# Optimization experiments

Measured on AMD Instinct MI355X. Metric: run time of the kernel, lower is better.

Reference implementation:

```python
import jax, jax.numpy as jnp
import numpy as np

N = 30000      # nodes
E = 480000     # edges per relation (avg degree 16)
H = 4          # GAT heads
D = 64         # out_size per head
F1, F2 = 256, 128   # per-metapath input feature dims
SIN = 256      # sen_in_size
HD = H * D     # 256, semantic-attention in_size
OUT = 64       # final out_size


def _gat(feat, src, dst, W, al, ar, b):
    """DGL GATConv (eval mode, dropout=0), activation=relu6."""
    h = (feat @ W).reshape(N, H, D)                     # [N,H,D]
    el = (h * al).sum(-1)                               # [N,H]
    er = (h * ar).sum(-1)                               # [N,H]
    e = jax.nn.leaky_relu(el[src] + er[dst], 0.2)       # [E,H]
    m = jax.ops.segment_max(e, dst, N)                  # edge-softmax over incoming edges
    p = jnp.exp(e - m[dst])
    s = jax.ops.segment_sum(p, dst, N)
    a = p / s[dst]                                      # [E,H]
    out = jax.ops.segment_sum(a[:, :, None] * h[src], dst, N)  # [N,H,D]
    out = out + b.reshape(1, H, D)
    return jnp.clip(out, 0.0, 6.0).reshape(N, H * D)    # relu6, flatten(1)


def _gcn_layer(x, src, dst, W, b):
    """DGL GraphConv, norm='both': D_in^{-1/2} A D_out^{-1/2} X W (+ b)."""
    ones = jnp.ones(src.shape[0], x.dtype)
    deg_o = jnp.clip(jax.ops.segment_sum(ones, src, N), 1.0, None)
    deg_i = jnp.clip(jax.ops.segment_sum(ones, dst, N), 1.0, None)
    h = (x @ W) * (deg_o[:, None] ** -0.5)
    h = jax.ops.segment_sum(h[src], dst, N) * (deg_i[:, None] ** -0.5)
    return h if b is None else h + b


def setup_inputs():
    key = jax.random.key(0)
    ks = jax.random.split(key, 28)
    f32 = jnp.float32
    nrm = lambda k, shp: jax.random.normal(k, shp, f32) * 0.05
    ri = lambda k, shp: jax.random.randint(k, shp, 0, N, jnp.int32)
    return dict(
        feat0=jax.random.normal(ks[0], (N, F1), f32),
        feat1=jax.random.normal(ks[1], (N, F2), f32),
        sen_feat=jax.random.normal(ks[2], (N, SIN), f32),
        Wgat0=nrm(ks[11], (F1, H * D)), al0=nrm(ks[12], (H, D)), ar0=nrm(ks[13], (H, D)), b0=nrm(ks[14], (H * D,)),
        Wgat1=nrm(ks[15], (F2, H * D)), al1=nrm(ks[16], (H, D)), ar1=nrm(ks[17], (H, D)), b1=nrm(ks[18], (H * D,)),
        Wp1=nrm(ks[19], (HD, OUT)), bp1=nrm(ks[20], (OUT,)), wp2=nrm(ks[21], (OUT,)),
        Wf=nrm(ks[22], (HD, OUT)), bf=nrm(ks[23], (OUT,)),
        Wg1=nrm(ks[24], (SIN, OUT)), bg1=nrm(ks[25], (OUT,)), Wg2=nrm(ks[26], (OUT, OUT)),
        src0=ri(ks[3], (E,)), dst0=ri(ks[4], (E,)),
        src1=ri(ks[5], (E,)), dst1=ri(ks[6], (E,)),
        gsrc=ri(ks[7], (E,)), gdst=ri(ks[8], (E,)),
        asrc=ri(ks[9], (E,)), adst=ri(ks[10], (E,)),
        k=10,
    )


def reference(feat0, feat1, sen_feat,
              Wgat0, al0, ar0, b0, Wgat1, al1, ar1, b1,
              Wp1, bp1, wp2, Wf, bf, Wg1, bg1, Wg2,
              src0, dst0, src1, dst1, gsrc, gdst, asrc, adst, k):
    # per-metapath GAT embeddings
    z0 = _gat(feat0, src0, dst0, Wgat0, al0, ar0, b0)   # [N, HD]
    z1 = _gat(feat1, src1, dst1, Wgat1, al1, ar1, b1)   # [N, HD]
    z = jnp.stack([z0, z1], axis=1)                     # [N, M=2, HD]
    # PathAttention (semantic attention over metapaths)
    w = jnp.tanh(z @ Wp1 + bp1) @ wp2                   # [N, M]
    beta = jax.nn.softmax(w.mean(0))                    # [M]
    fused = jnp.einsum('m,nmf->nf', beta, z)            # [N, HD]
    Femb = fused @ Wf + bf                              # [N, OUT]
    # two-layer GCN on the sentence graph
    p1 = jnp.tanh(_gcn_layer(sen_feat, gsrc, gdst, Wg1, bg1))
    P = _gcn_layer(p1, gsrc, gdst, Wg2, None)           # [N, OUT]
    # spectral loss: fuse embeddings, trace of Laplacian quadratic form on first k dims
    Z = 0.5 * (Femb + P)                                # [N, OUT]
    Zk = Z[:, :k]
    diff = Zk[asrc] - Zk[adst]
    tr = 0.5 * jnp.sum(diff * diff)                     # tr(Zk^T (D - A) Zk)
    return (tr, Z)
```

## Files before the change

kernel.cpp:

```cpp
#include <hip/hip_runtime.h>
#include <math.h>

#define NN 30000
#define NE 480000
#define NBLK 118
#define NMT 235
#define NTRB 7500
#define CAPD 128

typedef unsigned short ushort_t;
typedef unsigned int uint_t;
typedef __attribute__((ext_vector_type(8))) short short8;
typedef __attribute__((ext_vector_type(4))) float f32x4;

__device__ __forceinline__ ushort_t f2bf(float x) {
  uint_t u = __float_as_uint(x);
  u = (u + 0x7FFF + ((u >> 16) & 1)) >> 16;
  return (ushort_t)u;
}
__device__ __forceinline__ float bf2f(ushort_t v) {
  return __uint_as_float(((uint_t)v) << 16);
}

__device__ __forceinline__ float wred(float v) {
#pragma unroll
  for (int off = 32; off > 0; off >>= 1) v += __shfl_xor(v, off);
  return v;
}

__global__ void prep_kernel(float4* __restrict__ zp, const float* __restrict__ W0,
                            const float* __restrict__ W1, const float* __restrict__ W2,
                            const float* __restrict__ W3, const float* __restrict__ W4,
                            ushort_t* __restrict__ T0, ushort_t* __restrict__ T1,
                            ushort_t* __restrict__ T2, ushort_t* __restrict__ T3,
                            ushort_t* __restrict__ T4) {
  int id = blockIdx.x * 256 + threadIdx.x;
  if (id < 52501) {
    zp[id] = make_float4(0.f, 0.f, 0.f, 0.f);
    return;
  }
  int wid = id - 52501;
  const float* W;
  ushort_t* T;
  int K, N, base;
  if (wid < 65536) { W = W0; T = T0; K = 256; N = 256; base = 0; }
  else if (wid < 98304) { W = W1; T = T1; K = 128; N = 256; base = 65536; }
  else if (wid < 114688) { W = W2; T = T2; K = 256; N = 64; base = 98304; }
  else if (wid < 131072) { W = W3; T = T3; K = 256; N = 64; base = 114688; }
  else if (wid < 147456) { W = W4; T = T4; K = 256; N = 64; base = 131072; }
  else return;
  int l = wid - base;
  int k = l / N, n = l - k * N;
  T[(size_t)n * K + k] = f2bf(W[l]);
}


__device__ __forceinline__ void mfma_core_f32(const float* __restrict__ A0,
                                              const ushort_t* __restrict__ BT, int K, int bm,
                                              short* __restrict__ As, short* __restrict__ Bs,
                                              f32x4 acc[2][4]) {
  int tid = threadIdx.x;
  int lane = tid & 63, w = tid >> 6;
  int q = lane >> 4, mr = lane & 15;
#pragma unroll 1
  for (int k0 = 0; k0 < K; k0 += 32) {
    {
      int r = tid >> 1, hf = tid & 1;
      int gr = bm + r;
      float4 f0 = make_float4(0.f, 0.f, 0.f, 0.f), f1 = f0, f2 = f0, f3 = f0;
      if (gr < NN) {
        const float4* pa = (const float4*)(A0 + (size_t)gr * K + k0 + hf * 16);
        f0 = pa[0]; f1 = pa[1]; f2 = pa[2]; f3 = pa[3];
      }
      short8 lo, hi;
      lo[0] = (short)f2bf(f0.x); lo[1] = (short)f2bf(f0.y);
      lo[2] = (short)f2bf(f0.z); lo[3] = (short)f2bf(f0.w);
      lo[4] = (short)f2bf(f1.x); lo[5] = (short)f2bf(f1.y);
      lo[6] = (short)f2bf(f1.z); lo[7] = (short)f2bf(f1.w);
      hi[0] = (short)f2bf(f2.x); hi[1] = (short)f2bf(f2.y);
      hi[2] = (short)f2bf(f2.z); hi[3] = (short)f2bf(f2.w);
      hi[4] = (short)f2bf(f3.x); hi[5] = (short)f2bf(f3.y);
      hi[6] = (short)f2bf(f3.z); hi[7] = (short)f2bf(f3.w);
      short* dst = As + r * 40 + hf * 16;
      *(short8*)(dst) = lo;
      *(short8*)(dst + 8) = hi;
    }
    {
      int n = tid >> 2, qk = tid & 3;
      short8 bv = *(const short8*)((const short*)BT + (size_t)n * K + k0 + qk * 8);
      *(short8*)(Bs + n * 40 + qk * 8) = bv;
    }
    __syncthreads();
    short8 a0 = *(short8*)(As + (w * 32 + mr) * 40 + q * 8);
    short8 a1 = *(short8*)(As + (w * 32 + 16 + mr) * 40 + q * 8);
#pragma unroll
    for (int j = 0; j < 4; ++j) {
      short8 b = *(short8*)(Bs + (j * 16 + mr) * 40 + q * 8);
      acc[0][j] = __builtin_amdgcn_mfma_f32_16x16x32_bf16(a0, b, acc[0][j], 0, 0, 0);
      acc[1][j] = __builtin_amdgcn_mfma_f32_16x16x32_bf16(a1, b, acc[1][j], 0, 0, 0);
    }
    __syncthreads();
  }
}

__device__ __forceinline__ void mfma_core2_f32(const float* __restrict__ A0,
                                               const ushort_t* __restrict__ BT, int K, int bm,
                                               short* __restrict__ As, short* __restrict__ Bs,
                                               f32x4 acc[2][8]) {
  int tid = threadIdx.x;
  int lane = tid & 63, w = tid >> 6;
  int q = lane >> 4, mr = lane & 15;
#pragma unroll 1
  for (int k0 = 0; k0 < K; k0 += 32) {
    {
      int r = tid >> 1, hf = tid & 1;
      int gr = bm + r;
      float4 f0 = make_float4(0.f, 0.f, 0.f, 0.f), f1 = f0, f2 = f0, f3 = f0;
      if (gr < NN) {
        const float4* pa = (const float4*)(A0 + (size_t)gr * K + k0 + hf * 16);
        f0 = pa[0]; f1 = pa[1]; f2 = pa[2]; f3 = pa[3];
      }
      short8 lo, hi;
      lo[0] = (short)f2bf(f0.x); lo[1] = (short)f2bf(f0.y);
      lo[2] = (short)f2bf(f0.z); lo[3] = (short)f2bf(f0.w);
      lo[4] = (short)f2bf(f1.x); lo[5] = (short)f2bf(f1.y);
      lo[6] = (short)f2bf(f1.z); lo[7] = (short)f2bf(f1.w);
      hi[0] = (short)f2bf(f2.x); hi[1] = (short)f2bf(f2.y);
      hi[2] = (short)f2bf(f2.z); hi[3] = (short)f2bf(f2.w);
      hi[4] = (short)f2bf(f3.x); hi[5] = (short)f2bf(f3.y);
      hi[6] = (short)f2bf(f3.z); hi[7] = (short)f2bf(f3.w);
      short* dst = As + r * 40 + hf * 16;
      *(short8*)(dst) = lo;
      *(short8*)(dst + 8) = hi;
    }
    {
      int n = tid >> 1, qk = tid & 1;
      const short* src = (const short*)BT + (size_t)n * K + k0 + qk * 16;
      short8 b0 = *(const short8*)src;
      short8 b1 = *(const short8*)(src + 8);
      short* d = Bs + n * 40 + qk * 16;
      *(short8*)d = b0;
      *(short8*)(d + 8) = b1;
    }
    __syncthreads();
    short8 a0 = *(short8*)(As + (w * 32 + mr) * 40 + q * 8);
    short8 a1 = *(short8*)(As + (w * 32 + 16 + mr) * 40 + q * 8);
#pragma unroll
    for (int j = 0; j < 8; ++j) {
      short8 b = *(short8*)(Bs + (j * 16 + mr) * 40 + q * 8);
      acc[0][j] = __builtin_amdgcn_mfma_f32_16x16x32_bf16(a0, b, acc[0][j], 0, 0, 0);
      acc[1][j] = __builtin_amdgcn_mfma_f32_16x16x32_bf16(a1, b, acc[1][j], 0, 0, 0);
    }
    __syncthreads();
  }
}

__device__ __forceinline__ void mfma_core2_bf(const ushort_t* __restrict__ A0,
                                              const ushort_t* __restrict__ BT, int bm,
                                              short* __restrict__ As, short* __restrict__ Bs,
                                              f32x4 acc[2][8]) {
  int tid = threadIdx.x;
  int lane = tid & 63, w = tid >> 6;
  int q = lane >> 4, mr = lane & 15;
#pragma unroll 1
  for (int k0 = 0; k0 < 256; k0 += 32) {
    {
      int r = tid >> 1, hf = tid & 1;
      int gr = bm + r;
      short8 v0 = {0, 0, 0, 0, 0, 0, 0, 0}, v1 = v0;
      if (gr < NN) {
        const short* p0 = (const short*)A0 + (size_t)gr * 256 + k0 + hf * 16;
        v0 = *(const short8*)p0;
        v1 = *(const short8*)(p0 + 8);
      }
      short* dst = As + r * 40 + hf * 16;
      *(short8*)(dst) = v0;
      *(short8*)(dst + 8) = v1;
    }
    {
      int n = tid >> 1, qk = tid & 1;
      const short* src = (const short*)BT + (size_t)n * 256 + k0 + qk * 16;
      short8 b0 = *(const short8*)src;
      short8 b1 = *(const short8*)(src + 8);
      short* d = Bs + n * 40 + qk * 16;
      *(short8*)d = b0;
      *(short8*)(d + 8) = b1;
    }
    __syncthreads();
    short8 a0 = *(short8*)(As + (w * 32 + mr) * 40 + q * 8);
    short8 a1 = *(short8*)(As + (w * 32 + 16 + mr) * 40 + q * 8);
#pragma unroll
    for (int j = 0; j < 8; ++j) {
      short8 b = *(short8*)(Bs + (j * 16 + mr) * 40 + q * 8);
      acc[0][j] = __builtin_amdgcn_mfma_f32_16x16x32_bf16(a0, b, acc[0][j], 0, 0, 0);
      acc[1][j] = __builtin_amdgcn_mfma_f32_16x16x32_bf16(a1, b, acc[1][j], 0, 0, 0);
    }
    __syncthreads();
  }
}

__global__ __launch_bounds__(256) void mfma_all_kernel(
    const float* __restrict__ feat0, const float* __restrict__ feat1,
    const float* __restrict__ sen, const ushort_t* __restrict__ WT0,
    const ushort_t* __restrict__ WT1, const ushort_t* __restrict__ Wg1T,
    ushort_t* __restrict__ h0, ushort_t* __restrict__ h1, ushort_t* __restrict__ gcnA,
    const float* __restrict__ al0, const float* __restrict__ ar0, float* __restrict__ el0,
    float* __restrict__ er0, const float* __restrict__ al1, const float* __restrict__ ar1,
    float* __restrict__ el1, float* __restrict__ er1, const float* __restrict__ rdo) {
  __shared__ short As[128 * 40];
  __shared__ short Bs[128 * 40];
  int y = blockIdx.y;
  int bm = blockIdx.x * 128;
  int lane = threadIdx.x & 63, w = threadIdx.x >> 6;
  int q = lane >> 4, mr = lane & 15;
  if (y < 4) {
    int gsel = y >> 1, p = y & 1;
    const float* A = gsel ? feat1 : feat0;
    int K = gsel ? 128 : 256;
    const ushort_t* WT = gsel ? WT1 : WT0;
    ushort_t* H = gsel ? h1 : h0;
    const float* al = gsel ? al1 : al0;
    const float* ar = gsel ? ar1 : ar0;
    float* el = gsel ? el1 : el0;
    float* er = gsel ? er1 : er0;
    f32x4 acc[2][8];
#pragma unroll
    for (int i = 0; i < 2; ++i)
#pragma unroll
      for (int j = 0; j < 8; ++j) acc[i][j] = (f32x4){0.f, 0.f, 0.f, 0.f};
    mfma_core2_f32(A, WT + (size_t)p * 128 * K, K, bm, As, Bs, acc);
    float alv[8], arv[8];
#pragma unroll
    for (int j = 0; j < 8; ++j) {
      alv[j] = al[p * 128 + j * 16 + mr];
      arv[j] = ar[p * 128 + j * 16 + mr];
    }
#pragma unroll
    for (int i = 0; i < 2; ++i)
#pragma unroll
      for (int r = 0; r < 4; ++r) {
        int gr = bm + w * 32 + i * 16 + q * 4 + r;
        float pl0 = 0.f, pr0 = 0.f, pl1 = 0.f, pr1 = 0.f;
#pragma unroll
        for (int j = 0; j < 4; ++j) {
          pl0 = fmaf(acc[i][j][r], alv[j], pl0);
          pr0 = fmaf(acc[i][j][r], arv[j], pr0);
          pl1 = fmaf(acc[i][j + 4][r], alv[j + 4], pl1);
          pr1 = fmaf(acc[i][j + 4][r], arv[j + 4], pr1);
        }
#pragma unroll
        for (int m = 1; m < 16; m <<= 1) {
          pl0 += __shfl_xor(pl0, m);
          pr0 += __shfl_xor(pr0, m);
          pl1 += __shfl_xor(pl1, m);
          pr1 += __shfl_xor(pr1, m);
        }
        if (gr < NN) {
          if (mr == 0) {
            el[gr * 4 + 2 * p] = pl0;
            er[gr * 4 + 2 * p] = pr0;
            el[gr * 4 + 2 * p + 1] = pl1;
            er[gr * 4 + 2 * p + 1] = pr1;
          }
#pragma unroll
          for (int j = 0; j < 8; ++j)
            H[(size_t)gr * 256 + p * 128 + j * 16 + mr] = f2bf(acc[i][j][r]);
        }
      }
  } else {
    f32x4 acc[2][4];
#pragma unroll
    for (int i = 0; i < 2; ++i)
#pragma unroll
      for (int j = 0; j < 4; ++j) acc[i][j] = (f32x4){0.f, 0.f, 0.f, 0.f};
    mfma_core_f32(sen, Wg1T, 256, bm, As, Bs, acc);
#pragma unroll
    for (int i = 0; i < 2; ++i)
#pragma unroll
      for (int r = 0; r < 4; ++r) {
        int gr = bm + w * 32 + i * 16 + q * 4 + r;
        if (gr < NN) {
          float sc = rdo[gr];
#pragma unroll
          for (int j = 0; j < 4; ++j)
            gcnA[(size_t)gr * 64 + j * 16 + mr] = f2bf(acc[i][j][r] * sc);
        }
      }
  }
}

__global__ __launch_bounds__(256) void mfma_attnwf_kernel(
    const ushort_t* __restrict__ z0, const ushort_t* __restrict__ z1,
    const ushort_t* __restrict__ WpfT, const float* __restrict__ bp1,
    const float* __restrict__ wp2, float* __restrict__ pbuf, ushort_t* __restrict__ Y0,
    ushort_t* __restrict__ Y1) {
  __shared__ short As[128 * 40];
  __shared__ short Bs[128 * 40];
  __shared__ float wsum[4];
  const ushort_t* A = blockIdx.y ? z1 : z0;
  ushort_t* Y = blockIdx.y ? Y1 : Y0;
  int bm = blockIdx.x * 128;
  f32x4 acc[2][8];
#pragma unroll
  for (int i = 0; i < 2; ++i)
#pragma unroll
    for (int j = 0; j < 8; ++j) acc[i][j] = (f32x4){0.f, 0.f, 0.f, 0.f};
  mfma_core2_bf(A, WpfT, bm, As, Bs, acc);
  int lane = threadIdx.x & 63, w = threadIdx.x >> 6;
  int q = lane >> 4, mr = lane & 15;
  float local = 0.f;
#pragma unroll
  for (int j = 0; j < 4; ++j) {
    int col = j * 16 + mr;
    float bp = bp1[col], wp = wp2[col];
#pragma unroll
    for (int i = 0; i < 2; ++i)
#pragma unroll
      for (int r = 0; r < 4; ++r) {
        int gr = bm + w * 32 + i * 16 + q * 4 + r;
        if (gr < NN) local += tanhf(acc[i][j][r] + bp) * wp;
      }
  }
  local = wred(local);
  if (lane == 0) wsum[w] = local;
#pragma unroll
  for (int j = 4; j < 8; ++j) {
    int col = (j - 4) * 16 + mr;
#pragma unroll
    for (int i = 0; i < 2; ++i)
#pragma unroll
      for (int r = 0; r < 4; ++r) {
        int gr = bm + w * 32 + i * 16 + q * 4 + r;
        if (gr < NN) Y[(size_t)gr * 64 + col] = f2bf(acc[i][j][r]);
      }
  }
  __syncthreads();
  if (threadIdx.x == 0)
    pbuf[blockIdx.y * NMT + blockIdx.x] = wsum[0] + wsum[1] + wsum[2] + wsum[3];
}

__global__ void hist_kernel(const int* __restrict__ d0, const int* __restrict__ d1,
                            const int* __restrict__ d2, const int* __restrict__ d3,
                            int* __restrict__ cnt) {
  int g = blockIdx.y;
  const int* d = g == 0 ? d0 : g == 1 ? d1 : g == 2 ? d2 : d3;
  int e = blockIdx.x * 256 + threadIdx.x;
  if (e < NE) atomicAdd(&cnt[g * NN + d[e]], 1);
}

__global__ __launch_bounds__(256) void scan_blocks_kernel(const int* __restrict__ cnt,
                                                          int* __restrict__ rows,
                                                          int* __restrict__ bsum) {
  __shared__ int sm[256];
  int g = blockIdx.y, t = threadIdx.x;
  int i = blockIdx.x * 256 + t;
  int v = (i < NN) ? cnt[g * NN + i] : 0;
  sm[t] = v;
  __syncthreads();
#pragma unroll
  for (int off = 1; off < 256; off <<= 1) {
    int tmp = (t >= off) ? sm[t - off] : 0;
    __syncthreads();
    sm[t] += tmp;
    __syncthreads();
  }
  if (i < NN) rows[g * (NN + 1) + i] = sm[t] - v;
  if (t == 255) bsum[g * NBLK + blockIdx.x] = sm[255];
}

__global__ __launch_bounds__(128) void scan_tops_kernel(int* __restrict__ bsum,
                                                        int* __restrict__ boff) {
  __shared__ int sm[128];
  int g = blockIdx.y, t = threadIdx.x;
  int v = (t < NBLK) ? bsum[g * NBLK + t] : 0;
  sm[t] = v;
  __syncthreads();
#pragma unroll
  for (int off = 1; off < 128; off <<= 1) {
    int tmp = (t >= off) ? sm[t - off] : 0;
    __syncthreads();
    sm[t] += tmp;
    __syncthreads();
  }
  if (t < NBLK) boff[g * NBLK + t] = sm[t] - v;
}

__global__ void add_off_kernel(int* __restrict__ rows, const int* __restrict__ boff) {
  int g = blockIdx.y, t = threadIdx.x;
  int i = blockIdx.x * 256 + t;
  if (i < NN) rows[g * (NN + 1) + i] += boff[g * NBLK + blockIdx.x];
  if (blockIdx.x == 0 && t == 0) rows[g * (NN + 1) + NN] = NE;
}

__global__ void scatter_kernel(const int* __restrict__ s0, const int* __restrict__ s1,
                               const int* __restrict__ s2, const int* __restrict__ d0,
                               const int* __restrict__ d1, const int* __restrict__ d2,
                               const int* __restrict__ rows, int* __restrict__ cnt2,
                               int* __restrict__ cols, const int* __restrict__ cnt_deg,
                               float* __restrict__ rdo, float* __restrict__ rdi,
                               const int* __restrict__ rows_g) {
  int g = blockIdx.y;
  if (g == 3) {
    int n = blockIdx.x * 256 + threadIdx.x;
    if (n < NN) {
      rdo[n] = rsqrtf(fmaxf((float)cnt_deg[n], 1.f));
      float di = (float)(rows_g[n + 1] - rows_g[n]);
      rdi[n] = rsqrtf(fmaxf(di, 1.f));
    }
    return;
  }
  const int* sp = g == 0 ? s0 : g == 1 ? s1 : s2;
  const int* dp = g == 0 ? d0 : g == 1 ? d1 : d2;
  int e = blockIdx.x * 256 + threadIdx.x;
  if (e >= NE) return;
  int d = dp[e];
  int pos = rows[g * (NN + 1) + d] + atomicAdd(&cnt2[g * NN + d], 1);
  cols[(size_t)g * NE + pos] = sp[e];
}

__global__ __launch_bounds__(256) void gat_node_kernel(
    const int* __restrict__ rows0, const int* __restrict__ cols0, const float* __restrict__ el0,
    const float* __restrict__ er0, const ushort_t* __restrict__ h0,
    const float* __restrict__ bias0, ushort_t* __restrict__ zz0, const int* __restrict__ rows1,
    const int* __restrict__ cols1, const float* __restrict__ el1, const float* __restrict__ er1,
    const ushort_t* __restrict__ h1, const float* __restrict__ bias1,
    ushort_t* __restrict__ zz1) {
  __shared__ float aw[4][CAPD][4];
  int g = blockIdx.y;
  const int* rows = g ? rows1 : rows0;
  const int* cols = g ? cols1 : cols0;
  const float* el = g ? el1 : el0;
  const float* er = g ? er1 : er0;
  const ushort_t* h = g ? h1 : h0;
  const float* bias = g ? bias1 : bias0;
  ushort_t* z = g ? zz1 : zz0;

  int lane = threadIdx.x & 63, w = threadIdx.x >> 6;
  int n = blockIdx.x * 4 + w;
  int r0 = rows[n], r1 = rows[n + 1];
  int deg = r1 - r0;
  float4 er4 = *(const float4*)&er[n * 4];
  float s0 = 0.f, s1 = 0.f, s2 = 0.f, s3 = 0.f;
  for (int j = lane; j < deg; j += 64) {
    int s = cols[r0 + j];
    float4 elv = *(const float4*)&el[s * 4];
    float v0 = elv.x + er4.x; v0 = v0 > 0.f ? v0 : 0.2f * v0;
    float v1 = elv.y + er4.y; v1 = v1 > 0.f ? v1 : 0.2f * v1;
    float v2 = elv.z + er4.z; v2 = v2 > 0.f ? v2 : 0.2f * v2;
    float v3 = elv.w + er4.w; v3 = v3 > 0.f ? v3 : 0.2f * v3;
    float e0 = __expf(v0), e1 = __expf(v1), e2 = __expf(v2), e3 = __expf(v3);
    s0 += e0; s1 += e1; s2 += e2; s3 += e3;
    if (j < CAPD) {
      aw[w][j][0] = e0; aw[w][j][1] = e1; aw[w][j][2] = e2; aw[w][j][3] = e3;
    }
  }
  s0 = wred(s0); s1 = wred(s1); s2 = wred(s2); s3 = wred(s3);
  __syncthreads();
  int hh = lane >> 4;
  float denom = hh == 0 ? s0 : hh == 1 ? s1 : hh == 2 ? s2 : s3;
  float myer = hh == 0 ? er4.x : hh == 1 ? er4.y : hh == 2 ? er4.z : er4.w;
  float invd = (deg > 0) ? 1.f / denom : 0.f;
  float4 acc = make_float4(0.f, 0.f, 0.f, 0.f);
  int jc = deg < CAPD ? deg : CAPD;
  for (int j = 0; j < jc; j += 16) {
    int si[16];
    float ai[16];
#pragma unroll
    for (int t = 0; t < 16; ++t) {
      int jj = j + t;
      int jx = jj < jc ? jj : jc - 1;
      si[t] = cols[r0 + jx];
      ai[t] = (jj < jc) ? aw[w][jj][hh] : 0.f;
    }
    ushort4 ui[16];
#pragma unroll
    for (int t = 0; t < 16; ++t) ui[t] = *(const ushort4*)&h[(size_t)si[t] * 256 + lane * 4];
#pragma unroll
    for (int t = 0; t < 16; ++t) {
      acc.x = fmaf(ai[t], bf2f(ui[t].x), acc.x);
      acc.y = fmaf(ai[t], bf2f(ui[t].y), acc.y);
      acc.z = fmaf(ai[t], bf2f(ui[t].z), acc.z);
      acc.w = fmaf(ai[t], bf2f(ui[t].w), acc.w);
    }
  }
  for (int j = jc; j < deg; ++j) {
    int s = cols[r0 + j];
    float v = el[s * 4 + hh] + myer;
    v = v > 0.f ? v : 0.2f * v;
    float a = __expf(v);
    ushort4 hu = *(const ushort4*)&h[(size_t)s * 256 + lane * 4];
    acc.x = fmaf(a, bf2f(hu.x), acc.x);
    acc.y = fmaf(a, bf2f(hu.y), acc.y);
    acc.z = fmaf(a, bf2f(hu.z), acc.z);
    acc.w = fmaf(a, bf2f(hu.w), acc.w);
  }
  float4 bv = *(const float4*)&bias[lane * 4];
  ushort4 o;
  o.x = f2bf(fminf(fmaxf(acc.x * invd + bv.x, 0.f), 6.f));
  o.y = f2bf(fminf(fmaxf(acc.y * invd + bv.y, 0.f), 6.f));
  o.z = f2bf(fminf(fmaxf(acc.z * invd + bv.z, 0.f), 6.f));
  o.w = f2bf(fminf(fmaxf(acc.w * invd + bv.w, 0.f), 6.f));
  *(ushort4*)&z[(size_t)n * 256 + lane * 4] = o;
}

__global__ __launch_bounds__(256) void gcn_gather12_kernel(
    const int* __restrict__ rows, const int* __restrict__ cols, const ushort_t* __restrict__ X,
    const float* __restrict__ rdi, const float* __restrict__ bg1, const float* __restrict__ Wg2,
    const float* __restrict__ rdo, ushort_t* __restrict__ out2, const float* __restrict__ pbuf,
    float* __restrict__ wb) {
  __shared__ float psm[4][64];
  int lane = threadIdx.x & 63, w = threadIdx.x >> 6;
  if (blockIdx.x == 0) {
    __shared__ float sm[8];
    int t = threadIdx.x;
    float a0 = 0.f, a1 = 0.f;
    for (int i = t; i < NMT; i += 256) {
      a0 += pbuf[i];
      a1 += pbuf[NMT + i];
    }
    a0 = wred(a0);
    a1 = wred(a1);
    if (lane == 0) { sm[w] = a0; sm[4 + w] = a1; }
    __syncthreads();
    if (t == 0) {
      float w0 = (sm[0] + sm[1] + sm[2] + sm[3]) * (1.0f / NN);
      float w1 = (sm[4] + sm[5] + sm[6] + sm[7]) * (1.0f / NN);
      float mx = fmaxf(w0, w1);
      float e0 = expf(w0 - mx), e1 = expf(w1 - mx);
      float inv = 1.f / (e0 + e1);
      wb[2] = e0 * inv;
      wb[3] = e1 * inv;
    }
  }
  int n = blockIdx.x * 4 + w;
  if (n >= NN) return;
  int r0 = rows[n], r1 = rows[n + 1];
  int eg = lane >> 4, fl = lane & 15;
  float facc[4] = {0.f, 0.f, 0.f, 0.f};
  for (int j = r0; j < r1; j += 16) {
    int si[4];
    float sel[4];
#pragma unroll
    for (int t = 0; t < 4; ++t) {
      int jj = j + 4 * t + eg;
      int jx = jj < r1 ? jj : r1 - 1;
      si[t] = cols[jx];
      sel[t] = (jj < r1) ? 1.f : 0.f;
    }
    ushort4 xv[4];
#pragma unroll
    for (int t = 0; t < 4; ++t) xv[t] = *(const ushort4*)&X[(size_t)si[t] * 64 + fl * 4];
#pragma unroll
    for (int t = 0; t < 4; ++t) {
      facc[0] = fmaf(sel[t], bf2f(xv[t].x), facc[0]);
      facc[1] = fmaf(sel[t], bf2f(xv[t].y), facc[1]);
      facc[2] = fmaf(sel[t], bf2f(xv[t].z), facc[2]);
      facc[3] = fmaf(sel[t], bf2f(xv[t].w), facc[3]);
    }
  }
#pragma unroll
  for (int u = 0; u < 4; ++u) {
    facc[u] += __shfl_xor(facc[u], 16);
    facc[u] += __shfl_xor(facc[u], 32);
  }
  if (eg == 0) *(float4*)&psm[w][fl * 4] = make_float4(facc[0], facc[1], facc[2], facc[3]);
  __syncthreads();
  float p = tanhf(psm[w][lane] * rdi[n] + bg1[lane]);
  float o = 0.f;
#pragma unroll
  for (int k = 0; k < 64; ++k) o = fmaf(__shfl(p, k), Wg2[k * 64 + lane], o);
  out2[(size_t)n * 64 + lane] = f2bf(o * rdo[n]);
}

__global__ __launch_bounds__(256) void gcn_gather2_kernel(
    const int* __restrict__ rows, const int* __restrict__ cols, const ushort_t* __restrict__ X,
    const float* __restrict__ rdi, const ushort_t* __restrict__ Y0,
    const ushort_t* __restrict__ Y1, const float* __restrict__ wb, const float* __restrict__ bf,
    const int* __restrict__ kptr, float* __restrict__ Zc, float* __restrict__ dout) {
  int lane = threadIdx.x & 63, w = threadIdx.x >> 6;
  int n = blockIdx.x * 4 + w;
  if (n >= NN) return;
  int r0 = rows[n], r1 = rows[n + 1];
  int eg = lane >> 4, fl = lane & 15;
  float facc[4] = {0.f, 0.f, 0.f, 0.f};
  for (int j = r0; j < r1; j += 16) {
    int si[4];
    float sel[4];
#pragma unroll
    for (int t = 0; t < 4; ++t) {
      int jj = j + 4 * t + eg;
      int jx = jj < r1 ? jj : r1 - 1;
      si[t] = cols[jx];
      sel[t] = (jj < r1) ? 1.f : 0.f;
    }
    ushort4 xv[4];
#pragma unroll
    for (int t = 0; t < 4; ++t) xv[t] = *(const ushort4*)&X[(size_t)si[t] * 64 + fl * 4];
#pragma unroll
    for (int t = 0; t < 4; ++t) {
      facc[0] = fmaf(sel[t], bf2f(xv[t].x), facc[0]);
      facc[1] = fmaf(sel[t], bf2f(xv[t].y), facc[1]);
      facc[2] = fmaf(sel[t], bf2f(xv[t].z), facc[2]);
      facc[3] = fmaf(sel[t], bf2f(xv[t].w), facc[3]);
    }
  }
#pragma unroll
  for (int u = 0; u < 4; ++u) {
    facc[u] += __shfl_xor(facc[u], 16);
    facc[u] += __shfl_xor(facc[u], 32);
  }
  if (eg == 0) {
    float ri = rdi[n];
    ushort4 y0 = *(const ushort4*)&Y0[(size_t)n * 64 + fl * 4];
    ushort4 y1 = *(const ushort4*)&Y1[(size_t)n * 64 + fl * 4];
    float4 bfv = *(const float4*)&bf[fl * 4];
    float w2 = wb[2], w3 = wb[3];
    float zv[4];
    zv[0] = 0.5f * (w2 * bf2f(y0.x) + w3 * bf2f(y1.x) + bfv.x + facc[0] * ri);
    zv[1] = 0.5f * (w2 * bf2f(y0.y) + w3 * bf2f(y1.y) + bfv.y + facc[1] * ri);
    zv[2] = 0.5f * (w2 * bf2f(y0.z) + w3 * bf2f(y1.z) + bfv.z + facc[2] * ri);
    zv[3] = 0.5f * (w2 * bf2f(y0.w) + w3 * bf2f(y1.w) + bfv.w + facc[3] * ri);
    float* dp = dout + 1 + (size_t)n * 64 + fl * 4;
    dp[0] = zv[0]; dp[1] = zv[1]; dp[2] = zv[2]; dp[3] = zv[3];
    int k = *kptr;
    if (fl < 4) {
      float4 zk;
      zk.x = (fl * 4 + 0 < k) ? zv[0] : 0.f;
      zk.y = (fl * 4 + 1 < k) ? zv[1] : 0.f;
      zk.z = (fl * 4 + 2 < k) ? zv[2] : 0.f;
      zk.w = (fl * 4 + 3 < k) ? zv[3] : 0.f;
      *(float4*)&Zc[(size_t)n * 16 + fl * 4] = zk;
    }
  }
}

__global__ __launch_bounds__(256) void tr_kernel(const int* __restrict__ asrc,
                                                 const int* __restrict__ adst,
                                                 const int* __restrict__ kptr,
                                                 const float* __restrict__ Zc,
                                                 const float* __restrict__ dout,
                                                 float* __restrict__ trbuf) {
  __shared__ float wsum[4];
  int lane = threadIdx.x & 63, w = threadIdx.x >> 6;
  int k = *kptr;
  int eg = lane >> 2, c0 = (lane & 3) * 4;
  int e = blockIdx.x * 64 + w * 16 + eg;
  float local = 0.f;
  if (e < NE) {
    int a = asrc[e], b = adst[e];
    if (k <= 16) {
      float4 za = *(const float4*)&Zc[(size_t)a * 16 + c0];
      float4 zb = *(const float4*)&Zc[(size_t)b * 16 + c0];
      float dx = za.x - zb.x, dy = za.y - zb.y, dz = za.z - zb.z, dw = za.w - zb.w;
      local = dx * dx + dy * dy + dz * dz + dw * dw;
    } else {
      const float* Za = dout + 1 + (size_t)a * 64;
      const float* Zb = dout + 1 + (size_t)b * 64;
#pragma unroll
      for (int st = 0; st < 4; ++st) {
#pragma unroll
        for (int t = 0; t < 4; ++t) {
          int c = c0 + st * 16 + t;
          if (c < k) {
            float d2 = Za[c] - Zb[c];
            local += d2 * d2;
          }
        }
      }
    }
  }
#pragma unroll
  for (int off = 32; off > 0; off >>= 1) local += __shfl_down(local, off);
  if (lane == 0) wsum[w] = local;
  __syncthreads();
  if (threadIdx.x == 0) trbuf[blockIdx.x] = wsum[0] + wsum[1] + wsum[2] + wsum[3];
}

__global__ __launch_bounds__(256) void tr_reduce_kernel(const float* __restrict__ trbuf,
                                                        float* __restrict__ dout) {
  __shared__ float sm[4];
  int t = threadIdx.x;
  float a = 0.f;
  for (int i = t; i < NTRB; i += 256) a += trbuf[i];
  a = wred(a);
  int lane = t & 63, w = t >> 6;
  if (lane == 0) sm[w] = a;
  __syncthreads();
  if (t == 0) dout[0] = 0.5f * (sm[0] + sm[1] + sm[2] + sm[3]);
}

extern "C" void kernel_launch(void* const* d_in, const int* in_sizes, int n_in, void* d_out,
                              int out_size, void* d_ws, size_t ws_size, hipStream_t stream) {
  const float* feat0 = (const float*)d_in[0];
  const float* feat1 = (const float*)d_in[1];
  const float* sen = (const float*)d_in[2];
  const float* Wgat0 = (const float*)d_in[3];
  const float* al0 = (const float*)d_in[4];
  const float* ar0 = (const float*)d_in[5];
  const float* b0 = (const float*)d_in[6];
  const float* Wgat1 = (const float*)d_in[7];
  const float* al1 = (const float*)d_in[8];
  const float* ar1 = (const float*)d_in[9];
  const float* b1 = (const float*)d_in[10];
  const float* Wp1 = (const float*)d_in[11];
  const float* bp1 = (const float*)d_in[12];
  const float* wp2 = (const float*)d_in[13];
  const float* Wf = (const float*)d_in[14];
  const float* bf = (const float*)d_in[15];
  const float* Wg1 = (const float*)d_in[16];
  const float* bg1 = (const float*)d_in[17];
  const float* Wg2 = (const float*)d_in[18];
  const int* src0 = (const int*)d_in[19];
  const int* dst0 = (const int*)d_in[20];
  const int* src1 = (const int*)d_in[21];
  const int* dst1 = (const int*)d_in[22];
  const int* gsrc = (const int*)d_in[23];
  const int* gdst = (const int*)d_in[24];
  const int* asrc = (const int*)d_in[25];
  const int* adst = (const int*)d_in[26];
  const int* kptr = (const int*)d_in[27];
  float* out = (float*)d_out;
  float* ws = (float*)d_ws;

  float* wb = ws;
  int* cnt = (int*)(ws + 4);
  int* cnt2 = (int*)(ws + 120004);
  float* rdo = ws + 210004;
  float* rdi = ws + 240004;
  int* rows = (int*)(ws + 270004);
  int* bsum = (int*)(ws + 360008);
  int* boff = (int*)(ws + 360364);
  int* cols = (int*)(ws + 360720);
  float* el0 = ws + 1800720;
  float* er0 = ws + 1920720;
  float* el1 = ws + 2040720;
  float* er1 = ws + 2160720;
  float* pbuf = ws + 2280720;
  float* trbuf = el0;
  ushort_t* h0 = (ushort_t*)(ws + 2283068);
  ushort_t* h1 = (ushort_t*)(ws + 6123068);
  ushort_t* z0 = (ushort_t*)(ws + 9963068);
  ushort_t* z1 = (ushort_t*)(ws + 13803068);
  ushort_t* gcnA = (ushort_t*)(ws + 17643068);
  ushort_t* gcnA2 = (ushort_t*)(ws + 18603068);
  ushort_t* Y0 = (ushort_t*)(ws + 19563068);
  ushort_t* Y1 = (ushort_t*)(ws + 20523068);
  ushort_t* WT0 = (ushort_t*)(ws + 21483068);
  ushort_t* WT1 = (ushort_t*)(ws + 21515836);
  ushort_t* WpfT = (ushort_t*)(ws + 21532220);
  ushort_t* Wg1T = (ushort_t*)(ws + 21548604);
  float* Zc = ws + 21556796;

  int* rows_g = rows + 2 * (NN + 1);
  int* cols_g = cols + 2 * NE;
  int* cnt_deg = cnt + 3 * NN;

  prep_kernel<<<782, 256, 0, stream>>>((float4*)ws, Wgat0, Wgat1, Wp1, Wf, Wg1, WT0, WT1, WpfT,
                                       WpfT + 16384, Wg1T);

  hist_kernel<<<dim3(1875, 4), 256, 0, stream>>>(dst0, dst1, gdst, gsrc, cnt);
  scan_blocks_kernel<<<dim3(NBLK, 3), 256, 0, stream>>>(cnt, rows, bsum);
  scan_tops_kernel<<<dim3(1, 3), 128, 0, stream>>>(bsum, boff);
  add_off_kernel<<<dim3(NBLK, 3), 256, 0, stream>>>(rows, boff);
  scatter_kernel<<<dim3(1875, 4), 256, 0, stream>>>(src0, src1, gsrc, dst0, dst1, gdst, rows,
                                                    cnt2, cols, cnt_deg, rdo, rdi, rows_g);

  mfma_all_kernel<<<dim3(NMT, 5), 256, 0, stream>>>(feat0, feat1, sen, WT0, WT1, Wg1T, h0, h1,
                                                    gcnA, al0, ar0, el0, er0, al1, ar1, el1,
                                                    er1, rdo);

  gat_node_kernel<<<dim3(7500, 2), 256, 0, stream>>>(rows, cols, el0, er0, h0, b0, z0,
                                                     rows + (NN + 1), cols + NE, el1, er1, h1,
                                                     b1, z1);

  mfma_attnwf_kernel<<<dim3(NMT, 2), 256, 0, stream>>>(z0, z1, WpfT, bp1, wp2, pbuf, Y0, Y1);

  gcn_gather12_kernel<<<7500, 256, 0, stream>>>(rows_g, cols_g, gcnA, rdi, bg1, Wg2, rdo, gcnA2,
                                                pbuf, wb);
  gcn_gather2_kernel<<<7500, 256, 0, stream>>>(rows_g, cols_g, gcnA2, rdi, Y0, Y1, wb, bf, kptr,
                                               Zc, out);

  tr_kernel<<<NTRB, 256, 0, stream>>>(asrc, adst, kptr, Zc, out, trbuf);
  tr_reduce_kernel<<<1, 256, 0, stream>>>(trbuf, out);
}
```

Measured before the change: 515.9 us.

## Pre-convert GAT features to bf16, sort CSR neighbors, single-pass GAT aggregation

Measured after the change: 529.3 us. +2.6%, slower.

```diff
diff --git a/kernel.cpp b/kernel.cpp
--- a/kernel.cpp
+++ b/kernel.cpp
@@ -6,7 +6,6 @@
 #define NBLK 118
 #define NMT 235
 #define NTRB 7500
-#define CAPD 128
 
 typedef unsigned short ushort_t;
 typedef unsigned int uint_t;
@@ -33,25 +32,46 @@
                             const float* __restrict__ W3, const float* __restrict__ W4,
                             ushort_t* __restrict__ T0, ushort_t* __restrict__ T1,
                             ushort_t* __restrict__ T2, ushort_t* __restrict__ T3,
-                            ushort_t* __restrict__ T4) {
+                            ushort_t* __restrict__ T4, const float* __restrict__ F0,
+                            const float* __restrict__ F1, ushort_t* __restrict__ B0,
+                            ushort_t* __restrict__ B1) {
   int id = blockIdx.x * 256 + threadIdx.x;
   if (id < 52501) {
     zp[id] = make_float4(0.f, 0.f, 0.f, 0.f);
     return;
   }
   int wid = id - 52501;
-  const float* W;
-  ushort_t* T;
-  int K, N, base;
-  if (wid < 65536) { W = W0; T = T0; K = 256; N = 256; base = 0; }
-  else if (wid < 98304) { W = W1; T = T1; K = 128; N = 256; base = 65536; }
-  else if (wid < 114688) { W = W2; T = T2; K = 256; N = 64; base = 98304; }
-  else if (wid < 131072) { W = W3; T = T3; K = 256; N = 64; base = 114688; }
-  else if (wid < 147456) { W = W4; T = T4; K = 256; N = 64; base = 131072; }
-  else return;
-  int l = wid - base;
-  int k = l / N, n = l - k * N;
-  T[(size_t)n * K + k] = f2bf(W[l]);
+  if (wid < 147456) {
+    const float* W;
+    ushort_t* T;
+    int K, N, base;
+    if (wid < 65536) { W = W0; T = T0; K = 256; N = 256; base = 0; }
+    else if (wid < 98304) { W = W1; T = T1; K = 128; N = 256; base = 65536; }
+    else if (wid < 114688) { W = W2; T = T2; K = 256; N = 64; base = 98304; }
+    else if (wid < 131072) { W = W3; T = T3; K = 256; N = 64; base = 114688; }
+    else { W = W4; T = T4; K = 256; N = 64; base = 131072; }
+    int l = wid - base;
+    int k = l / N, n = l - k * N;
+    T[(size_t)n * K + k] = f2bf(W[l]);
+    return;
+  }
+  int cid = wid - 147456;
+  const float* S;
+  ushort_t* D;
+  if (cid < 960000) { S = F0; D = B0; }
+  else {
+    cid -= 960000;
+    if (cid >= 480000) return;
+    S = F1; D = B1;
+  }
+  const float4* p = (const float4*)(S + (size_t)cid * 8);
+  float4 a = p[0], b = p[1];
+  short8 o;
+  o[0] = (short)f2bf(a.x); o[1] = (short)f2bf(a.y);
+  o[2] = (short)f2bf(a.z); o[3] = (short)f2bf(a.w);
+  o[4] = (short)f2bf(b.x); o[5] = (short)f2bf(b.y);
+  o[6] = (short)f2bf(b.z); o[7] = (short)f2bf(b.w);
+  *(short8*)(D + (size_t)cid * 8) = o;
 }
 
 
@@ -103,7 +123,7 @@
   }
 }
 
-__device__ __forceinline__ void mfma_core2_f32(const float* __restrict__ A0,
+__device__ __forceinline__ void mfma_core2_bfK(const ushort_t* __restrict__ A0,
                                                const ushort_t* __restrict__ BT, int K, int bm,
                                                short* __restrict__ As, short* __restrict__ Bs,
                                                f32x4 acc[2][8]) {
@@ -115,23 +135,15 @@
     {
       int r = tid >> 1, hf = tid & 1;
       int gr = bm + r;
-      float4 f0 = make_float4(0.f, 0.f, 0.f, 0.f), f1 = f0, f2 = f0, f3 = f0;
+      short8 v0 = {0, 0, 0, 0, 0, 0, 0, 0}, v1 = v0;
       if (gr < NN) {
-        const float4* pa = (const float4*)(A0 + (size_t)gr * K + k0 + hf * 16);
-        f0 = pa[0]; f1 = pa[1]; f2 = pa[2]; f3 = pa[3];
+        const short* p0 = (const short*)A0 + (size_t)gr * K + k0 + hf * 16;
+        v0 = *(const short8*)p0;
+        v1 = *(const short8*)(p0 + 8);
       }
-      short8 lo, hi;
-      lo[0] = (short)f2bf(f0.x); lo[1] = (short)f2bf(f0.y);
-      lo[2] = (short)f2bf(f0.z); lo[3] = (short)f2bf(f0.w);
-      lo[4] = (short)f2bf(f1.x); lo[5] = (short)f2bf(f1.y);
-      lo[6] = (short)f2bf(f1.z); lo[7] = (short)f2bf(f1.w);
-      hi[0] = (short)f2bf(f2.x); hi[1] = (short)f2bf(f2.y);
-      hi[2] = (short)f2bf(f2.z); hi[3] = (short)f2bf(f2.w);
-      hi[4] = (short)f2bf(f3.x); hi[5] = (short)f2bf(f3.y);
-      hi[6] = (short)f2bf(f3.z); hi[7] = (short)f2bf(f3.w);
       short* dst = As + r * 40 + hf * 16;
-      *(short8*)(dst) = lo;
-      *(short8*)(dst + 8) = hi;
+      *(short8*)(dst) = v0;
+      *(short8*)(dst + 8) = v1;
     }
     {
       int n = tid >> 1, qk = tid & 1;
@@ -155,52 +167,8 @@
   }
 }
 
-__device__ __forceinline__ void mfma_core2_bf(const ushort_t* __restrict__ A0,
-                                              const ushort_t* __restrict__ BT, int bm,
-                                              short* __restrict__ As, short* __restrict__ Bs,
-                                              f32x4 acc[2][8]) {
-  int tid = threadIdx.x;
-  int lane = tid & 63, w = tid >> 6;
-  int q = lane >> 4, mr = lane & 15;
-#pragma unroll 1
-  for (int k0 = 0; k0 < 256; k0 += 32) {
-    {
-      int r = tid >> 1, hf = tid & 1;
-      int gr = bm + r;
-      short8 v0 = {0, 0, 0, 0, 0, 0, 0, 0}, v1 = v0;
-      if (gr < NN) {
-        const short* p0 = (const short*)A0 + (size_t)gr * 256 + k0 + hf * 16;
-        v0 = *(const short8*)p0;
-        v1 = *(const short8*)(p0 + 8);
-      }
-      short* dst = As + r * 40 + hf * 16;
-      *(short8*)(dst) = v0;
-      *(short8*)(dst + 8) = v1;
-    }
-    {
-      int n = tid >> 1, qk = tid & 1;
-      const short* src = (const short*)BT + (size_t)n * 256 + k0 + qk * 16;
-      short8 b0 = *(const short8*)src;
-      short8 b1 = *(const short8*)(src + 8);
-      short* d = Bs + n * 40 + qk * 16;
-      *(short8*)d = b0;
-      *(short8*)(d + 8) = b1;
-    }
-    __syncthreads();
-    short8 a0 = *(short8*)(As + (w * 32 + mr) * 40 + q * 8);
-    short8 a1 = *(short8*)(As + (w * 32 + 16 + mr) * 40 + q * 8);
-#pragma unroll
-    for (int j = 0; j < 8; ++j) {
-      short8 b = *(short8*)(Bs + (j * 16 + mr) * 40 + q * 8);
-      acc[0][j] = __builtin_amdgcn_mfma_f32_16x16x32_bf16(a0, b, acc[0][j], 0, 0, 0);
-      acc[1][j] = __builtin_amdgcn_mfma_f32_16x16x32_bf16(a1, b, acc[1][j], 0, 0, 0);
-    }
-    __syncthreads();
-  }
-}
-
 __global__ __launch_bounds__(256) void mfma_all_kernel(
-    const float* __restrict__ feat0, const float* __restrict__ feat1,
+    const ushort_t* __restrict__ fB0, const ushort_t* __restrict__ fB1,
     const float* __restrict__ sen, const ushort_t* __restrict__ WT0,
     const ushort_t* __restrict__ WT1, const ushort_t* __restrict__ Wg1T,
     ushort_t* __restrict__ h0, ushort_t* __restrict__ h1, ushort_t* __restrict__ gcnA,
@@ -215,7 +183,7 @@
   int q = lane >> 4, mr = lane & 15;
   if (y < 4) {
     int gsel = y >> 1, p = y & 1;
-    const float* A = gsel ? feat1 : feat0;
+    const ushort_t* A = gsel ? fB1 : fB0;
     int K = gsel ? 128 : 256;
     const ushort_t* WT = gsel ? WT1 : WT0;
     ushort_t* H = gsel ? h1 : h0;
@@ -228,7 +196,7 @@
     for (int i = 0; i < 2; ++i)
 #pragma unroll
       for (int j = 0; j < 8; ++j) acc[i][j] = (f32x4){0.f, 0.f, 0.f, 0.f};
-    mfma_core2_f32(A, WT + (size_t)p * 128 * K, K, bm, As, Bs, acc);
+    mfma_core2_bfK(A, WT + (size_t)p * 128 * K, K, bm, As, Bs, acc);
     float alv[8], arv[8];
 #pragma unroll
     for (int j = 0; j < 8; ++j) {
@@ -305,7 +273,7 @@
   for (int i = 0; i < 2; ++i)
 #pragma unroll
     for (int j = 0; j < 8; ++j) acc[i][j] = (f32x4){0.f, 0.f, 0.f, 0.f};
-  mfma_core2_bf(A, WpfT, bm, As, Bs, acc);
+  mfma_core2_bfK(A, WpfT, 256, bm, As, Bs, acc);
   int lane = threadIdx.x & 63, w = threadIdx.x >> 6;
   int q = lane >> 4, mr = lane & 15;
   float local = 0.f;
@@ -418,6 +386,36 @@
   cols[(size_t)g * NE + pos] = sp[e];
 }
 
+__global__ __launch_bounds__(256) void sort_kernel(const int* __restrict__ rows0,
+                                                   int* __restrict__ cols0,
+                                                   const int* __restrict__ rows1,
+                                                   int* __restrict__ cols1) {
+  int g = blockIdx.y;
+  const int* rows = g ? rows1 : rows0;
+  int* cols = g ? cols1 : cols0;
+  int lane = threadIdx.x & 63, w = threadIdx.x >> 6;
+  int half = lane >> 5, ll = lane & 31;
+  int n = blockIdx.x * 8 + w * 2 + half;
+  if (n >= NN) return;
+  int r0 = rows[n], r1 = rows[n + 1];
+  int deg = r1 - r0;
+  if (deg < 2 || deg > 32) return;
+  int v = (ll < deg) ? cols[r0 + ll] : 0x7FFFFFFF;
+#pragma unroll
+  for (int k = 2; k <= 32; k <<= 1) {
+#pragma unroll
+    for (int j = k >> 1; j > 0; j >>= 1) {
+      int o = __shfl_xor(v, j);
+      bool up = ((ll & k) == 0);
+      bool lower = ((ll & j) == 0);
+      int mn = v < o ? v : o;
+      int mx = v < o ? o : v;
+      v = (up == lower) ? mn : mx;
+    }
+  }
+  if (ll < deg) cols[r0 + ll] = v;
+}
+
 __global__ __launch_bounds__(256) void gat_node_kernel(
     const int* __restrict__ rows0, const int* __restrict__ cols0, const float* __restrict__ el0,
     const float* __restrict__ er0, const ushort_t* __restrict__ h0,
@@ -425,7 +423,6 @@
     const int* __restrict__ cols1, const float* __restrict__ el1, const float* __restrict__ er1,
     const ushort_t* __restrict__ h1, const float* __restrict__ bias1,
     ushort_t* __restrict__ zz1) {
-  __shared__ float aw[4][CAPD][4];
   int g = blockIdx.y;
   const int* rows = g ? rows1 : rows0;
   const int* cols = g ? cols1 : cols0;
@@ -437,63 +434,41 @@
 
   int lane = threadIdx.x & 63, w = threadIdx.x >> 6;
   int n = blockIdx.x * 4 + w;
+  int hh = lane >> 4;
+  float4 er4 = *(const float4*)&er[n * 4];
+  float myer = hh == 0 ? er4.x : hh == 1 ? er4.y : hh == 2 ? er4.z : er4.w;
   int r0 = rows[n], r1 = rows[n + 1];
   int deg = r1 - r0;
-  float4 er4 = *(const float4*)&er[n * 4];
-  float s0 = 0.f, s1 = 0.f, s2 = 0.f, s3 = 0.f;
-  for (int j = lane; j < deg; j += 64) {
-    int s = cols[r0 + j];
-    float4 elv = *(const float4*)&el[s * 4];
-    float v0 = elv.x + er4.x; v0 = v0 > 0.f ? v0 : 0.2f * v0;
-    float v1 = elv.y + er4.y; v1 = v1 > 0.f ? v1 : 0.2f * v1;
-    float v2 = elv.z + er4.z; v2 = v2 > 0.f ? v2 : 0.2f * v2;
-    float v3 = elv.w + er4.w; v3 = v3 > 0.f ? v3 : 0.2f * v3;
-    float e0 = __expf(v0), e1 = __expf(v1), e2 = __expf(v2), e3 = __expf(v3);
-    s0 += e0; s1 += e1; s2 += e2; s3 += e3;
-    if (j < CAPD) {
-      aw[w][j][0] = e0; aw[w][j][1] = e1; aw[w][j][2] = e2; aw[w][j][3] = e3;
-    }
-  }
-  s0 = wred(s0); s1 = wred(s1); s2 = wred(s2); s3 = wred(s3);
-  __syncthreads();
-  int hh = lane >> 4;
-  float denom = hh == 0 ? s0 : hh == 1 ? s1 : hh == 2 ? s2 : s3;
-  float myer = hh == 0 ? er4.x : hh == 1 ? er4.y : hh == 2 ? er4.z : er4.w;
-  float invd = (deg > 0) ? 1.f / denom : 0.f;
+  float ssum = 0.f;
   float4 acc = make_float4(0.f, 0.f, 0.f, 0.f);
-  int jc = deg < CAPD ? deg : CAPD;
-  for (int j = 0; j < jc; j += 16) {
+  for (int j = 0; j < deg; j += 16) {
     int si[16];
-    float ai[16];
 #pragma unroll
     for (int t = 0; t < 16; ++t) {
       int jj = j + t;
-      int jx = jj < jc ? jj : jc - 1;
+      int jx = jj < deg ? jj : deg - 1;
       si[t] = cols[r0 + jx];
-      ai[t] = (jj < jc) ? aw[w][jj][hh] : 0.f;
-    }
-    ushort4 ui[16];
-#pragma unroll
-    for (int t = 0; t < 16; ++t) ui[t] = *(const ushort4*)&h[(size_t)si[t] * 256 + lane * 4];
+    }
+    float ev[16];
+#pragma unroll
+    for (int t = 0; t < 16; ++t) ev[t] = el[si[t] * 4 + hh];
+    ushort4 hv[16];
+#pragma unroll
+    for (int t = 0; t < 16; ++t) hv[t] = *(const ushort4*)&h[(size_t)si[t] * 256 + lane * 4];
 #pragma unroll
     for (int t = 0; t < 16; ++t) {
-      acc.x = fmaf(ai[t], bf2f(ui[t].x), acc.x);
-      acc.y = fmaf(ai[t], bf2f(ui[t].y), acc.y);
-      acc.z = fmaf(ai[t], bf2f(ui[t].z), acc.z);
-      acc.w = fmaf(ai[t], bf2f(ui[t].w), acc.w);
-    }
-  }
-  for (int j = jc; j < deg; ++j) {
-    int s = cols[r0 + j];
-    float v = el[s * 4 + hh] + myer;
-    v = v > 0.f ? v : 0.2f * v;
-    float a = __expf(v);
-    ushort4 hu = *(const ushort4*)&h[(size_t)s * 256 + lane * 4];
-    acc.x = fmaf(a, bf2f(hu.x), acc.x);
-    acc.y = fmaf(a, bf2f(hu.y), acc.y);
-    acc.z = fmaf(a, bf2f(hu.z), acc.z);
-    acc.w = fmaf(a, bf2f(hu.w), acc.w);
-  }
+      float v = ev[t] + myer;
+      v = v > 0.f ? v : 0.2f * v;
+      float e = __expf(v);
+      e = (j + t < deg) ? e : 0.f;
+      ssum += e;
+      acc.x = fmaf(e, bf2f(hv[t].x), acc.x);
+      acc.y = fmaf(e, bf2f(hv[t].y), acc.y);
+      acc.z = fmaf(e, bf2f(hv[t].z), acc.z);
+      acc.w = fmaf(e, bf2f(hv[t].w), acc.w);
+    }
+  }
+  float invd = (deg > 0) ? 1.f / ssum : 0.f;
   float4 bv = *(const float4*)&bias[lane * 4];
   ushort4 o;
   o.x = f2bf(fminf(fmaxf(acc.x * invd + bv.x, 0.f), 6.f));
@@ -755,8 +730,11 @@
   int* cols_g = cols + 2 * NE;
   int* cnt_deg = cnt + 3 * NN;
 
-  prep_kernel<<<782, 256, 0, stream>>>((float4*)ws, Wgat0, Wgat1, Wp1, Wf, Wg1, WT0, WT1, WpfT,
-                                       WpfT + 16384, Wg1T);
+  ushort_t* fB0 = z0;
+  ushort_t* fB1 = z1;
+
+  prep_kernel<<<6407, 256, 0, stream>>>((float4*)ws, Wgat0, Wgat1, Wp1, Wf, Wg1, WT0, WT1, WpfT,
+                                        WpfT + 16384, Wg1T, feat0, feat1, fB0, fB1);
 
   hist_kernel<<<dim3(1875, 4), 256, 0, stream>>>(dst0, dst1, gdst, gsrc, cnt);
   scan_blocks_kernel<<<dim3(NBLK, 3), 256, 0, stream>>>(cnt, rows, bsum);
@@ -765,7 +743,9 @@
   scatter_kernel<<<dim3(1875, 4), 256, 0, stream>>>(src0, src1, gsrc, dst0, dst1, gdst, rows,
                                                     cnt2, cols, cnt_deg, rdo, rdi, rows_g);
 
-  mfma_all_kernel<<<dim3(NMT, 5), 256, 0, stream>>>(feat0, feat1, sen, WT0, WT1, Wg1T, h0, h1,
+  sort_kernel<<<dim3(3750, 2), 256, 0, stream>>>(rows, cols, rows + (NN + 1), cols + NE);
+
+  mfma_all_kernel<<<dim3(NMT, 5), 256, 0, stream>>>(fB0, fB1, sen, WT0, WT1, Wg1T, h0, h1,
                                                     gcnA, al0, ar0, el0, er0, al1, ar1, el1,
                                                     er1, rdo);
 
```
